# Performance work log

Hardware: AMD Instinct MI355X
Metric: run time of the kernel (lower is better)

Reference implementation:

```python
import jax, jax.numpy as jnp
import numpy as np

FREQUENCY_COUNT = 16

def setup_inputs() -> dict:
    key = jax.random.key(0)
    k1, k2 = jax.random.split(key)
    x = jax.random.normal(k1, (4096, 1024), dtype=jnp.float32)
    coef = jax.random.normal(k2, (1024, 1024, 2 * FREQUENCY_COUNT + 1), dtype=jnp.float32) * 0.1
    return {"x": x, "coef": coef}

def _fourier_features(x, K):
    ks = jnp.arange(1, K + 1, dtype=x.dtype)            # [K]
    ang = x[:, :, None] * ks[None, None, :]             # [B, I, K]
    ones = jnp.ones(x.shape + (1,), dtype=x.dtype)      # [B, I, 1]
    return jnp.concatenate([jnp.sin(ang), jnp.cos(ang), ones], axis=2)

def reference(x, coef):
    K = (coef.shape[-1] - 1) // 2
    values = _fourier_features(x, K)                     # [B, I, 2K+1]
    # sum over input dim i and frequency dim k, weighted per output j
    return jnp.einsum("oik,bik->bo", coef, values)      # [B, O]
```

## Files before the change

kernel.cpp:

```cpp
#include <hip/hip_runtime.h>


#define B_ROWS 4096
#define O_COLS 1024
#define I_DIM  1024
#define NF     33
#define NIB    16
#define KPRIME (NIB * NF * 64)
#define CW_ELEMS ((size_t)O_COLS * (size_t)KPRIME)

typedef _Float16 half8 __attribute__((ext_vector_type(8)));
typedef float float4v __attribute__((ext_vector_type(4)));

union H8 { half8 v; _Float16 h[8]; };

__device__ __forceinline__ void gload16(const void* g, void* l) {
  typedef const __attribute__((address_space(1))) unsigned int GU;
  typedef __attribute__((address_space(3))) unsigned int LU;
  __builtin_amdgcn_global_load_lds((GU*)g, (LU*)l, 16, 0, 0);
}

__device__ __forceinline__ int ksrc_of(int f) {
  return (f == 32) ? 32 : ((f >> 1) + ((f & 1) ? 16 : 0));
}

__global__ __launch_bounds__(64)
void convert_coef(const float* __restrict__ coef, _Float16* __restrict__ Cw) {
  const int bid = blockIdx.x;
  const int o = bid >> 4;
  const int ib = bid & 15;
  const int j = threadIdx.x;
  const int i = ib * 64 + j;

  const float* src = coef + (size_t)o * (I_DIM * NF) + (size_t)i * NF;
  float r[NF];
#pragma unroll
  for (int kk = 0; kk < NF; ++kk) r[kk] = src[kk];

  const int c = j >> 3, e = j & 7;
  const int jswz = ((c ^ (o & 7)) << 3) + e;
  _Float16* dst = Cw + (size_t)o * KPRIME + (size_t)ib * (NF * 64) + jswz;
#pragma unroll
  for (int f = 0; f < NF; ++f) {
    dst[f * 64] = (_Float16)r[ksrc_of(f)];
  }
}

template <bool USE_WS>
__global__ __launch_bounds__(512, 2)
void fourier_gemm(const float* __restrict__ x, const float* __restrict__ coef,
                  const _Float16* __restrict__ Cw, float* __restrict__ out) {
  __shared__ _Float16 As[128 * 64];
  __shared__ _Float16 Bs[128 * 64];

  const int tid = threadIdx.x;
  const int lane = tid & 63;
  const int wave = tid >> 6;
  const int wr = wave >> 1;
  const int wc = wave & 1;

  const int bid = blockIdx.x;
  const int o0 = (bid & 7) * 128;
  const int m0 = (bid >> 3) * 128;

  const int rowA = tid >> 3;
  const int rowB = rowA + 64;
  const int cch = tid & 7;
  const int cswz = cch ^ (rowA & 7);

  const int n1 = tid >> 3;
  const int n2 = n1 + 64;
  const int c1q = tid & 7;

  float4v acc[2][4] = {};

  float s1a[8], c1a[8], sa[8], ca[8];
  float s1b[8], c1b[8], sb[8], cb[8];

  const int r16 = lane & 15;
  const int kq = lane >> 4;

  for (int ib = 0; ib < NIB; ++ib) {
    {
      const float* xa = x + (size_t)(m0 + rowA) * I_DIM + ib * 64 + cch * 8;
      const float* xb = x + (size_t)(m0 + rowB) * I_DIM + ib * 64 + cch * 8;
      float xva[8], xvb[8];
      *(float4*)&xva[0] = *(const float4*)(xa);
      *(float4*)&xva[4] = *(const float4*)(xa + 4);
      *(float4*)&xvb[0] = *(const float4*)(xb);
      *(float4*)&xvb[4] = *(const float4*)(xb + 4);
#pragma unroll
      for (int e = 0; e < 8; ++e) {
        __sincosf(xva[e], &s1a[e], &c1a[e]);
        sa[e] = s1a[e]; ca[e] = c1a[e];
        __sincosf(xvb[e], &s1b[e], &c1b[e]);
        sb[e] = s1b[e]; cb[e] = c1b[e];
      }
    }

#pragma unroll 1
    for (int f = 0; f < NF; ++f) {
      H8 ha, hb;
      if (f == 32) {
#pragma unroll
        for (int e = 0; e < 8; ++e) { ha.h[e] = (_Float16)1.0f; hb.h[e] = (_Float16)1.0f; }
      } else if ((f & 1) == 0) {
#pragma unroll
        for (int e = 0; e < 8; ++e) { ha.h[e] = (_Float16)sa[e]; hb.h[e] = (_Float16)sb[e]; }
      } else {
#pragma unroll
        for (int e = 0; e < 8; ++e) { ha.h[e] = (_Float16)ca[e]; hb.h[e] = (_Float16)cb[e]; }
      }

      __syncthreads();

      *(half8*)&As[rowA * 64 + cswz * 8] = ha.v;
      *(half8*)&As[rowB * 64 + cswz * 8] = hb.v;

      if (USE_WS) {
        const _Float16* sp = Cw + (size_t)(o0 + n1) * KPRIME
                               + (size_t)ib * (NF * 64) + f * 64 + c1q * 8;
        gload16(sp, (char*)Bs + wave * 1024);
        gload16(sp + (size_t)64 * KPRIME, (char*)Bs + 8192 + wave * 1024);
      } else {
        const int ks = ksrc_of(f);
        H8 b1, b2;
#pragma unroll
        for (int e = 0; e < 8; ++e) {
          const size_t ii = (size_t)(ib * 64 + c1q * 8 + e) * NF + ks;
          b1.h[e] = (_Float16)coef[(size_t)(o0 + n1) * (I_DIM * NF) + ii];
          b2.h[e] = (_Float16)coef[(size_t)(o0 + n2) * (I_DIM * NF) + ii];
        }
        const int cs = (c1q ^ (n1 & 7)) << 3;
        *(half8*)&Bs[n1 * 64 + cs] = b1.v;
        *(half8*)&Bs[n2 * 64 + cs] = b2.v;
      }

      if (f & 1) {
#pragma unroll
        for (int e = 0; e < 8; ++e) {
          float ns = sa[e] * c1a[e] + ca[e] * s1a[e];
          ca[e] = ca[e] * c1a[e] - sa[e] * s1a[e];
          sa[e] = ns;
          float nsb = sb[e] * c1b[e] + cb[e] * s1b[e];
          cb[e] = cb[e] * c1b[e] - sb[e] * s1b[e];
          sb[e] = nsb;
        }
      }

      __syncthreads();

#pragma unroll
      for (int ksu = 0; ksu < 2; ++ksu) {
        const int ch = ((ksu << 2) + kq) ^ (r16 & 7);
        half8 af[2], bf[4];
#pragma unroll
        for (int fr = 0; fr < 2; ++fr)
          af[fr] = *(const half8*)&As[(wr * 32 + fr * 16 + r16) * 64 + ch * 8];
#pragma unroll
        for (int fc = 0; fc < 4; ++fc)
          bf[fc] = *(const half8*)&Bs[(wc * 64 + fc * 16 + r16) * 64 + ch * 8];
#pragma unroll
        for (int fr = 0; fr < 2; ++fr)
#pragma unroll
          for (int fc = 0; fc < 4; ++fc)
            acc[fr][fc] = __builtin_amdgcn_mfma_f32_16x16x32_f16(
                af[fr], bf[fc], acc[fr][fc], 0, 0, 0);
      }
    }
  }

#pragma unroll
  for (int fr = 0; fr < 2; ++fr)
#pragma unroll
    for (int fc = 0; fc < 4; ++fc)
#pragma unroll
      for (int r = 0; r < 4; ++r) {
        const int row = m0 + wr * 32 + fr * 16 + kq * 4 + r;
        const int col = o0 + wc * 64 + fc * 16 + r16;
        out[(size_t)row * O_COLS + col] = acc[fr][fc][r];
      }
}

extern "C" void kernel_launch(void* const* d_in, const int* in_sizes, int n_in,
                              void* d_out, int out_size, void* d_ws, size_t ws_size,
                              hipStream_t stream) {
  const float* x = (const float*)d_in[0];
  const float* coef = (const float*)d_in[1];
  float* out = (float*)d_out;
  _Float16* Cw = (_Float16*)d_ws;

  const bool use_ws = ws_size >= CW_ELEMS * sizeof(_Float16);

  if (use_ws) {
    convert_coef<<<dim3(O_COLS * NIB), dim3(64), 0, stream>>>(coef, Cw);
    fourier_gemm<true><<<dim3(256), dim3(512), 0, stream>>>(x, coef, Cw, out);
  } else {
    fourier_gemm<false><<<dim3(256), dim3(512), 0, stream>>>(x, coef, Cw, out);
  }
}
```

Measured before the change: 475.6 us.

## Double-buffer LDS tiles to overlap next-step staging with MFMA compute

Shared memory for the A and B tiles is doubled so the next frequency step's coefficient load (global_load_lds) and the sin/cos feature generation are issued into the alternate buffer before the current step's MFMAs run. This cuts one of the two barriers per step and lets the global-load latency overlap with compute. In exchange, LDS use doubles to 64 KB per block, which with two blocks per CU may limit occupancy, and the async LDS loads now rely on the single trailing barrier for completion ordering.

```diff
diff --git a/kernel.cpp b/kernel.cpp
--- a/kernel.cpp
+++ b/kernel.cpp
@@ -50,8 +50,8 @@
 __global__ __launch_bounds__(512, 2)
 void fourier_gemm(const float* __restrict__ x, const float* __restrict__ coef,
                   const _Float16* __restrict__ Cw, float* __restrict__ out) {
-  __shared__ _Float16 As[128 * 64];
-  __shared__ _Float16 Bs[128 * 64];
+  __shared__ _Float16 As[2][128 * 64];
+  __shared__ _Float16 Bs[2][128 * 64];
 
   const int tid = threadIdx.x;
   const int lane = tid & 63;
@@ -64,91 +64,104 @@
   const int m0 = (bid >> 3) * 128;
 
   const int rowA = tid >> 3;
-  const int rowB = rowA + 64;
   const int cch = tid & 7;
   const int cswz = cch ^ (rowA & 7);
 
   const int n1 = tid >> 3;
-  const int n2 = n1 + 64;
   const int c1q = tid & 7;
+
+  const int r16 = lane & 15;
+  const int kq = lane >> 4;
 
   float4v acc[2][4] = {};
 
   float s1a[8], c1a[8], sa[8], ca[8];
   float s1b[8], c1b[8], sb[8], cb[8];
 
-  const int r16 = lane & 15;
-  const int kq = lane >> 4;
-
+  const float* xa_base = x + (size_t)(m0 + rowA) * I_DIM + cch * 8;
+  const float* xb_base = xa_base + (size_t)64 * I_DIM;
+
+  auto init_ib = [&](int ib) {
+    float xva[8], xvb[8];
+    *(float4*)&xva[0] = *(const float4*)(xa_base + ib * 64);
+    *(float4*)&xva[4] = *(const float4*)(xa_base + ib * 64 + 4);
+    *(float4*)&xvb[0] = *(const float4*)(xb_base + ib * 64);
+    *(float4*)&xvb[4] = *(const float4*)(xb_base + ib * 64 + 4);
+#pragma unroll
+    for (int e = 0; e < 8; ++e) {
+      __sincosf(xva[e], &s1a[e], &c1a[e]);
+      sa[e] = s1a[e]; ca[e] = c1a[e];
+      __sincosf(xvb[e], &s1b[e], &c1b[e]);
+      sb[e] = s1b[e]; cb[e] = c1b[e];
+    }
+  };
+
+  auto stage_A = [&](int f1, int pn) {
+    H8 ha, hb;
+    if (f1 == NF - 1) {
+#pragma unroll
+      for (int e = 0; e < 8; ++e) { ha.h[e] = (_Float16)1.0f; hb.h[e] = (_Float16)1.0f; }
+    } else if ((f1 & 1) == 0) {
+#pragma unroll
+      for (int e = 0; e < 8; ++e) { ha.h[e] = (_Float16)sa[e]; hb.h[e] = (_Float16)sb[e]; }
+    } else {
+#pragma unroll
+      for (int e = 0; e < 8; ++e) { ha.h[e] = (_Float16)ca[e]; hb.h[e] = (_Float16)cb[e]; }
+    }
+    *(half8*)&As[pn][rowA * 64 + cswz * 8] = ha.v;
+    *(half8*)&As[pn][(rowA + 64) * 64 + cswz * 8] = hb.v;
+    if ((f1 & 1) && f1 < NF - 1) {
+#pragma unroll
+      for (int e = 0; e < 8; ++e) {
+        float ns = sa[e] * c1a[e] + ca[e] * s1a[e];
+        ca[e] = ca[e] * c1a[e] - sa[e] * s1a[e];
+        sa[e] = ns;
+        float nsb = sb[e] * c1b[e] + cb[e] * s1b[e];
+        cb[e] = cb[e] * c1b[e] - sb[e] * s1b[e];
+        sb[e] = nsb;
+      }
+    }
+  };
+
+  auto stage_B = [&](int ib1, int f1, int pn) {
+    if (USE_WS) {
+      const _Float16* sp = Cw + (size_t)(o0 + n1) * KPRIME
+                             + (size_t)ib1 * (NF * 64) + f1 * 64 + c1q * 8;
+      gload16(sp, (char*)&Bs[pn][0] + wave * 1024);
+      gload16(sp + (size_t)64 * KPRIME, (char*)&Bs[pn][0] + 8192 + wave * 1024);
+    } else {
+      const int ks = ksrc_of(f1);
+      H8 b1, b2;
+#pragma unroll
+      for (int e = 0; e < 8; ++e) {
+        const size_t ii = (size_t)(ib1 * 64 + c1q * 8 + e) * NF + ks;
+        b1.h[e] = (_Float16)coef[(size_t)(o0 + n1) * (I_DIM * NF) + ii];
+        b2.h[e] = (_Float16)coef[(size_t)(o0 + n1 + 64) * (I_DIM * NF) + ii];
+      }
+      const int cs = (c1q ^ (n1 & 7)) << 3;
+      *(half8*)&Bs[pn][n1 * 64 + cs] = b1.v;
+      *(half8*)&Bs[pn][(n1 + 64) * 64 + cs] = b2.v;
+    }
+  };
+
+  init_ib(0);
+  stage_B(0, 0, 0);
+  stage_A(0, 0);
+  __syncthreads();
+
+  int p = 0;
+#pragma unroll 1
   for (int ib = 0; ib < NIB; ++ib) {
-    {
-      const float* xa = x + (size_t)(m0 + rowA) * I_DIM + ib * 64 + cch * 8;
-      const float* xb = x + (size_t)(m0 + rowB) * I_DIM + ib * 64 + cch * 8;
-      float xva[8], xvb[8];
-      *(float4*)&xva[0] = *(const float4*)(xa);
-      *(float4*)&xva[4] = *(const float4*)(xa + 4);
-      *(float4*)&xvb[0] = *(const float4*)(xb);
-      *(float4*)&xvb[4] = *(const float4*)(xb + 4);
-#pragma unroll
-      for (int e = 0; e < 8; ++e) {
-        __sincosf(xva[e], &s1a[e], &c1a[e]);
-        sa[e] = s1a[e]; ca[e] = c1a[e];
-        __sincosf(xvb[e], &s1b[e], &c1b[e]);
-        sb[e] = s1b[e]; cb[e] = c1b[e];
-      }
-    }
-
 #pragma unroll 1
     for (int f = 0; f < NF; ++f) {
-      H8 ha, hb;
-      if (f == 32) {
-#pragma unroll
-        for (int e = 0; e < 8; ++e) { ha.h[e] = (_Float16)1.0f; hb.h[e] = (_Float16)1.0f; }
-      } else if ((f & 1) == 0) {
-#pragma unroll
-        for (int e = 0; e < 8; ++e) { ha.h[e] = (_Float16)sa[e]; hb.h[e] = (_Float16)sb[e]; }
-      } else {
-#pragma unroll
-        for (int e = 0; e < 8; ++e) { ha.h[e] = (_Float16)ca[e]; hb.h[e] = (_Float16)cb[e]; }
-      }
-
-      __syncthreads();
-
-      *(half8*)&As[rowA * 64 + cswz * 8] = ha.v;
-      *(half8*)&As[rowB * 64 + cswz * 8] = hb.v;
-
-      if (USE_WS) {
-        const _Float16* sp = Cw + (size_t)(o0 + n1) * KPRIME
-                               + (size_t)ib * (NF * 64) + f * 64 + c1q * 8;
-        gload16(sp, (char*)Bs + wave * 1024);
-        gload16(sp + (size_t)64 * KPRIME, (char*)Bs + 8192 + wave * 1024);
-      } else {
-        const int ks = ksrc_of(f);
-        H8 b1, b2;
-#pragma unroll
-        for (int e = 0; e < 8; ++e) {
-          const size_t ii = (size_t)(ib * 64 + c1q * 8 + e) * NF + ks;
-          b1.h[e] = (_Float16)coef[(size_t)(o0 + n1) * (I_DIM * NF) + ii];
-          b2.h[e] = (_Float16)coef[(size_t)(o0 + n2) * (I_DIM * NF) + ii];
-        }
-        const int cs = (c1q ^ (n1 & 7)) << 3;
-        *(half8*)&Bs[n1 * 64 + cs] = b1.v;
-        *(half8*)&Bs[n2 * 64 + cs] = b2.v;
-      }
-
-      if (f & 1) {
-#pragma unroll
-        for (int e = 0; e < 8; ++e) {
-          float ns = sa[e] * c1a[e] + ca[e] * s1a[e];
-          ca[e] = ca[e] * c1a[e] - sa[e] * s1a[e];
-          sa[e] = ns;
-          float nsb = sb[e] * c1b[e] + cb[e] * s1b[e];
-          cb[e] = cb[e] * c1b[e] - sb[e] * s1b[e];
-          sb[e] = nsb;
-        }
-      }
-
-      __syncthreads();
+      if (f < NF - 1) {
+        stage_B(ib, f + 1, p ^ 1);
+        stage_A(f + 1, p ^ 1);
+      } else if (ib < NIB - 1) {
+        stage_B(ib + 1, 0, p ^ 1);
+        init_ib(ib + 1);
+        stage_A(0, p ^ 1);
+      }
 
 #pragma unroll
       for (int ksu = 0; ksu < 2; ++ksu) {
@@ -156,10 +169,10 @@
         half8 af[2], bf[4];
 #pragma unroll
         for (int fr = 0; fr < 2; ++fr)
-          af[fr] = *(const half8*)&As[(wr * 32 + fr * 16 + r16) * 64 + ch * 8];
+          af[fr] = *(const half8*)&As[p][(wr * 32 + fr * 16 + r16) * 64 + ch * 8];
 #pragma unroll
         for (int fc = 0; fc < 4; ++fc)
-          bf[fc] = *(const half8*)&Bs[(wc * 64 + fc * 16 + r16) * 64 + ch * 8];
+          bf[fc] = *(const half8*)&Bs[p][(wc * 64 + fc * 16 + r16) * 64 + ch * 8];
 #pragma unroll
         for (int fr = 0; fr < 2; ++fr)
 #pragma unroll
@@ -167,6 +180,9 @@
             acc[fr][fc] = __builtin_amdgcn_mfma_f32_16x16x32_f16(
                 af[fr], bf[fc], acc[fr][fc], 0, 0, 0);
       }
+
+      __syncthreads();
+      p ^= 1;
     }
   }
 
```

Result: no change. 469.6 us (-1.3%).

## Split-K GEMM across two blocks, fold constant term into precomputed bias

Applied to the files above, without the earlier changes.

Splits the input-dim reduction into two halves, so 512 blocks run instead of 256. Each block writes its partial sums with atomicAdd into an output zeroed beforehand. The constant-feature column is dropped from the GEMM: its coefficients are reduced into a per-output bias during conversion and used to initialise the accumulators of one split. Occupancy hint raised to 4 blocks per CU and the feature loop unrolled by 2. The cost is an extra memset, float atomics with nondeterministic summation order, and slightly more register pressure.

```diff
diff --git a/kernel.cpp b/kernel.cpp
--- a/kernel.cpp
+++ b/kernel.cpp
@@ -1,17 +1,16 @@
 #include <hip/hip_runtime.h>
 
 
-#define B_ROWS 4096
 #define O_COLS 1024
 #define I_DIM  1024
-#define NF     33
+#define NFW    32
+#define NF33   33
 #define NIB    16
-#define KPRIME (NIB * NF * 64)
-#define CW_ELEMS ((size_t)O_COLS * (size_t)KPRIME)
+#define KPW    (NIB * NFW * 64)
+#define CW_BYTES ((size_t)O_COLS * KPW * 2)
 
 typedef _Float16 half8 __attribute__((ext_vector_type(8)));
 typedef float float4v __attribute__((ext_vector_type(4)));
-
 union H8 { half8 v; _Float16 h[8]; };
 
 __device__ __forceinline__ void gload16(const void* g, void* l) {
@@ -21,35 +20,42 @@
 }
 
 __device__ __forceinline__ int ksrc_of(int f) {
-  return (f == 32) ? 32 : ((f >> 1) + ((f & 1) ? 16 : 0));
+  return (f >= 32) ? 32 : ((f >> 1) + ((f & 1) ? 16 : 0));
 }
 
 __global__ __launch_bounds__(64)
-void convert_coef(const float* __restrict__ coef, _Float16* __restrict__ Cw) {
+void convert_coef(const float* __restrict__ coef, _Float16* __restrict__ Cw,
+                  float* __restrict__ bias) {
   const int bid = blockIdx.x;
   const int o = bid >> 4;
   const int ib = bid & 15;
   const int j = threadIdx.x;
   const int i = ib * 64 + j;
 
-  const float* src = coef + (size_t)o * (I_DIM * NF) + (size_t)i * NF;
-  float r[NF];
-#pragma unroll
-  for (int kk = 0; kk < NF; ++kk) r[kk] = src[kk];
+  const float* src = coef + (size_t)o * (I_DIM * NF33) + (size_t)i * NF33;
+  float r[NF33];
+#pragma unroll
+  for (int kk = 0; kk < NF33; ++kk) r[kk] = src[kk];
 
   const int c = j >> 3, e = j & 7;
   const int jswz = ((c ^ (o & 7)) << 3) + e;
-  _Float16* dst = Cw + (size_t)o * KPRIME + (size_t)ib * (NF * 64) + jswz;
-#pragma unroll
-  for (int f = 0; f < NF; ++f) {
+  _Float16* dst = Cw + (size_t)o * KPW + (size_t)ib * (NFW * 64) + jswz;
+#pragma unroll
+  for (int f = 0; f < NFW; ++f) {
     dst[f * 64] = (_Float16)r[ksrc_of(f)];
   }
+
+  float bsum = r[32];
+#pragma unroll
+  for (int off = 32; off > 0; off >>= 1) bsum += __shfl_down(bsum, off);
+  if (j == 0) atomicAdd(&bias[o], bsum);
 }
 
 template <bool USE_WS>
-__global__ __launch_bounds__(512, 2)
+__global__ __launch_bounds__(512, 4)
 void fourier_gemm(const float* __restrict__ x, const float* __restrict__ coef,
-                  const _Float16* __restrict__ Cw, float* __restrict__ out) {
+                  const _Float16* __restrict__ Cw, const float* __restrict__ bias,
+                  float* __restrict__ out) {
   __shared__ _Float16 As[128 * 64];
   __shared__ _Float16 Bs[128 * 64];
 
@@ -61,29 +67,48 @@
 
   const int bid = blockIdx.x;
   const int o0 = (bid & 7) * 128;
-  const int m0 = (bid >> 3) * 128;
+  const int kb = (bid >> 3) & 1;
+  const int m0 = (bid >> 4) * 128;
 
   const int rowA = tid >> 3;
-  const int rowB = rowA + 64;
   const int cch = tid & 7;
   const int cswz = cch ^ (rowA & 7);
 
   const int n1 = tid >> 3;
-  const int n2 = n1 + 64;
   const int c1q = tid & 7;
 
-  float4v acc[2][4] = {};
+  const int r16 = lane & 15;
+  const int kq = lane >> 4;
+
+  const int NFG = USE_WS ? NFW : NF33;
+
+  float4v acc[2][4];
+#pragma unroll
+  for (int fr = 0; fr < 2; ++fr)
+#pragma unroll
+    for (int fc = 0; fc < 4; ++fc)
+      acc[fr][fc] = (float4v){0.f, 0.f, 0.f, 0.f};
+  if (USE_WS && kb == 0) {
+#pragma unroll
+    for (int fc = 0; fc < 4; ++fc) {
+      const float bv = bias[o0 + wc * 64 + fc * 16 + r16];
+      acc[0][fc] = (float4v){bv, bv, bv, bv};
+      acc[1][fc] = acc[0][fc];
+    }
+  }
 
   float s1a[8], c1a[8], sa[8], ca[8];
   float s1b[8], c1b[8], sb[8], cb[8];
 
-  const int r16 = lane & 15;
-  const int kq = lane >> 4;
-
-  for (int ib = 0; ib < NIB; ++ib) {
+  const float* xa_base = x + (size_t)(m0 + rowA) * I_DIM + (size_t)kb * 512 + cch * 8;
+  const float* xb_base = xa_base + (size_t)64 * I_DIM;
+  const _Float16* spB = Cw + (size_t)(o0 + n1) * KPW + (size_t)kb * 8 * (NFW * 64) + c1q * 8;
+
+#pragma unroll 1
+  for (int ib2 = 0; ib2 < 8; ++ib2) {
     {
-      const float* xa = x + (size_t)(m0 + rowA) * I_DIM + ib * 64 + cch * 8;
-      const float* xb = x + (size_t)(m0 + rowB) * I_DIM + ib * 64 + cch * 8;
+      const float* xa = xa_base + ib2 * 64;
+      const float* xb = xb_base + ib2 * 64;
       float xva[8], xvb[8];
       *(float4*)&xva[0] = *(const float4*)(xa);
       *(float4*)&xva[4] = *(const float4*)(xa + 4);
@@ -98,10 +123,10 @@
       }
     }
 
-#pragma unroll 1
-    for (int f = 0; f < NF; ++f) {
+#pragma unroll 2
+    for (int f = 0; f < NFG; ++f) {
       H8 ha, hb;
-      if (f == 32) {
+      if (!USE_WS && f == 32) {
 #pragma unroll
         for (int e = 0; e < 8; ++e) { ha.h[e] = (_Float16)1.0f; hb.h[e] = (_Float16)1.0f; }
       } else if ((f & 1) == 0) {
@@ -114,29 +139,29 @@
 
       __syncthreads();
 
-      *(half8*)&As[rowA * 64 + cswz * 8] = ha.v;
-      *(half8*)&As[rowB * 64 + cswz * 8] = hb.v;
-
       if (USE_WS) {
-        const _Float16* sp = Cw + (size_t)(o0 + n1) * KPRIME
-                               + (size_t)ib * (NF * 64) + f * 64 + c1q * 8;
-        gload16(sp, (char*)Bs + wave * 1024);
-        gload16(sp + (size_t)64 * KPRIME, (char*)Bs + 8192 + wave * 1024);
+        gload16(spB, (char*)Bs + wave * 1024);
+        gload16(spB + (size_t)64 * KPW, (char*)Bs + 8192 + wave * 1024);
+        spB += 64;
       } else {
         const int ks = ksrc_of(f);
+        const int ibg = kb * 8 + ib2;
         H8 b1, b2;
 #pragma unroll
         for (int e = 0; e < 8; ++e) {
-          const size_t ii = (size_t)(ib * 64 + c1q * 8 + e) * NF + ks;
-          b1.h[e] = (_Float16)coef[(size_t)(o0 + n1) * (I_DIM * NF) + ii];
-          b2.h[e] = (_Float16)coef[(size_t)(o0 + n2) * (I_DIM * NF) + ii];
+          const size_t ii = (size_t)(ibg * 64 + c1q * 8 + e) * NF33 + ks;
+          b1.h[e] = (_Float16)coef[(size_t)(o0 + n1) * (I_DIM * NF33) + ii];
+          b2.h[e] = (_Float16)coef[(size_t)(o0 + n1 + 64) * (I_DIM * NF33) + ii];
         }
         const int cs = (c1q ^ (n1 & 7)) << 3;
         *(half8*)&Bs[n1 * 64 + cs] = b1.v;
-        *(half8*)&Bs[n2 * 64 + cs] = b2.v;
-      }
-
-      if (f & 1) {
+        *(half8*)&Bs[(n1 + 64) * 64 + cs] = b2.v;
+      }
+
+      *(half8*)&As[rowA * 64 + cswz * 8] = ha.v;
+      *(half8*)&As[(rowA + 64) * 64 + cswz * 8] = hb.v;
+
+      if ((f & 1) && (f + 2 < NFG)) {
 #pragma unroll
         for (int e = 0; e < 8; ++e) {
           float ns = sa[e] * c1a[e] + ca[e] * s1a[e];
@@ -178,7 +203,7 @@
       for (int r = 0; r < 4; ++r) {
         const int row = m0 + wr * 32 + fr * 16 + kq * 4 + r;
         const int col = o0 + wc * 64 + fc * 16 + r16;
-        out[(size_t)row * O_COLS + col] = acc[fr][fc][r];
+        atomicAdd(&out[(size_t)row * O_COLS + col], acc[fr][fc][r]);
       }
 }
 
@@ -188,14 +213,18 @@
   const float* x = (const float*)d_in[0];
   const float* coef = (const float*)d_in[1];
   float* out = (float*)d_out;
-  _Float16* Cw = (_Float16*)d_ws;
-
-  const bool use_ws = ws_size >= CW_ELEMS * sizeof(_Float16);
+
+  const bool use_ws = ws_size >= CW_BYTES + O_COLS * sizeof(float);
+
+  hipMemsetAsync(d_out, 0, (size_t)4096 * O_COLS * sizeof(float), stream);
 
   if (use_ws) {
-    convert_coef<<<dim3(O_COLS * NIB), dim3(64), 0, stream>>>(coef, Cw);
-    fourier_gemm<true><<<dim3(256), dim3(512), 0, stream>>>(x, coef, Cw, out);
+    _Float16* Cw = (_Float16*)d_ws;
+    float* bias = (float*)((char*)d_ws + CW_BYTES);
+    hipMemsetAsync(bias, 0, O_COLS * sizeof(float), stream);
+    convert_coef<<<dim3(O_COLS * NIB), dim3(64), 0, stream>>>(coef, Cw, bias);
+    fourier_gemm<true><<<dim3(512), dim3(512), 0, stream>>>(x, coef, Cw, bias, out);
   } else {
-    fourier_gemm<false><<<dim3(256), dim3(512), 0, stream>>>(x, coef, Cw, out);
-  }
-}
+    fourier_gemm<false><<<dim3(512), dim3(512), 0, stream>>>(x, coef, nullptr, nullptr, out);
+  }
+}
```

Measured after the change: 409.5 us. 1.16x faster.
